# Kernel tuning notes

Measured on AMD Instinct MI355X. Metric: run time of the kernel, lower is better.

## Reference

```python
import jax, jax.numpy as jnp
import numpy as np


def setup_inputs() -> dict:
    key = jax.random.key(0)
    ks = jax.random.split(key, 20)
    r = lambda i, shape: jax.random.normal(ks[i], shape, dtype=jnp.float32)
    return {
        "cli": r(0, (1, 1, 8)),
        "conv1_w": r(1, (1,)), "conv1_b": r(2, (1,)),
        "conv2_w": r(3, (1,)), "conv2_b": r(4, (1,)),
        "mlp1_w1": r(5, (32, 8)) * 0.3, "mlp1_b1": r(6, (32,)) * 1e-6,
        "mlp1_w2": r(7, (8, 32)) * 0.3, "mlp1_b2": r(8, (8,)) * 1e-6,
        "mlp2_w1": r(9, (32, 8)) * 0.3, "mlp2_b1": r(10, (32,)) * 1e-6,
        "mlp2_w2": r(11, (8, 32)) * 0.3, "mlp2_b2": r(12, (8,)) * 1e-6,
        "gcn1_w": r(13, (1,)), "gcn1_b": r(14, (1,)),
        "gcn2_w": r(15, (1,)), "gcn2_b": r(16, (1,)),
    }


def _mlp(x, w1, b1, w2, b2):
    # torch nn.Linear: y = x @ W.T + b ; exact (erf) GELU; dropout is identity in eval.
    h = jax.nn.gelu(x @ w1.T + b1, approximate=False)
    return h @ w2.T + b2


def reference(cli, conv1_w, conv1_b, conv2_w, conv2_b,
              mlp1_w1, mlp1_b1, mlp1_w2, mlp1_b2,
              mlp2_w1, mlp2_b1, mlp2_w2, mlp2_b2,
              gcn1_w, gcn1_b, gcn2_w, gcn2_b):
    # Conv1d(1,1,1) == scalar affine transform.
    sigma = cli * conv1_w + conv1_b                     # [1,1,8]
    sigma_out = sigma.reshape(1, 8, 1) @ sigma          # [1,8,8] outer product

    x = cli[0]                                          # [1,8]
    cli_ss = _mlp(x, mlp1_w1, mlp1_b1, mlp1_w2, mlp1_b2).reshape(1, 1, 8)
    cli_mm = _mlp(x, mlp2_w1, mlp2_b1, mlp2_w2, mlp2_b2).reshape(1, 8, 1)

    diag_cha = cli_mm @ cli_ss                          # [1,8,8]
    diag_att = diag_cha * sigma_out                     # [1,8,8]

    alpha = cli * conv2_w + conv2_b                     # [1,1,8]
    alpha_T = alpha.reshape(1, 8, 1)
    similarity_c = (diag_cha @ alpha_T) @ alpha         # [1,8,8]
    similarity = jax.nn.softmax(similarity_c + diag_att, axis=1)

    # GCN(num_state=1): seg stays [1,1,8]
    seg = jax.nn.relu(cli * gcn1_w + gcn1_b)            # [1,1,8]
    seg_similar = seg @ similarity                      # [1,1,8]
    out = jax.nn.relu(seg_similar * gcn2_w + gcn2_b)
    return (out + seg)[:, 0, :]                         # squeeze(1) -> [1,8]
```

## Files before the change

kernel.cpp:

```cpp
#include <hip/hip_runtime.h>
#include <math.h>

__device__ __forceinline__ float gelu_exact(float x) {
    return 0.5f * x * (1.0f + erff(x * 0.70710678118654752440f));
}

__global__ void __launch_bounds__(64) clngcn_fused(
    const float* __restrict__ cli,
    const float* __restrict__ c1w, const float* __restrict__ c1b,
    const float* __restrict__ c2w, const float* __restrict__ c2b,
    const float* __restrict__ m1w1, const float* __restrict__ m1b1,
    const float* __restrict__ m1w2, const float* __restrict__ m1b2,
    const float* __restrict__ m2w1, const float* __restrict__ m2b1,
    const float* __restrict__ m2w2, const float* __restrict__ m2b2,
    const float* __restrict__ g1w, const float* __restrict__ g1b,
    const float* __restrict__ g2w, const float* __restrict__ g2b,
    float* __restrict__ out)
{
    const int t = threadIdx.x;
    const int i = t >> 3;
    const int j = t & 7;
    const int k = t & 31;
    const bool lo = (t < 32);

    float x[8];
    #pragma unroll
    for (int q = 0; q < 8; ++q) x[q] = cli[q];

    const float C1W = c1w[0], C1B = c1b[0];
    const float C2W = c2w[0], C2B = c2b[0];
    const float G1W = g1w[0], G1B = g1b[0];
    const float G2W = g2w[0], G2B = g2b[0];

    const float* W1 = lo ? m1w1 : m2w1;
    const float* B1 = lo ? m1b1 : m2b1;
    const float* W2 = lo ? m1w2 : m2w2;
    const float* B2 = lo ? m1b2 : m2b2;

    float acc = B1[k];
    #pragma unroll
    for (int q = 0; q < 8; ++q) acc = fmaf(x[q], W1[k * 8 + q], acc);
    const float h = gelu_exact(acc);

    float r[8];
    #pragma unroll
    for (int q = 0; q < 8; ++q) {
        float p = h * W2[q * 32 + k];
        p += __shfl_xor(p, 1);
        p += __shfl_xor(p, 2);
        p += __shfl_xor(p, 4);
        p += __shfl_xor(p, 8);
        p += __shfl_xor(p, 16);
        r[q] = p + B2[q];
    }
    float cs[8], cm[8];
    #pragma unroll
    for (int q = 0; q < 8; ++q) {
        const float o = __shfl_xor(r[q], 32);
        cs[q] = lo ? r[q] : o;
        cm[q] = lo ? o : r[q];
    }

    const float sigma_i = fmaf(x[i], C1W, C1B);
    const float sigma_j = fmaf(x[j], C1W, C1B);
    const float alpha_j = fmaf(x[j], C2W, C2B);
    const float seg_i   = fmaxf(fmaf(x[i], G1W, G1B), 0.0f);
    const float seg_j   = fmaxf(fmaf(x[j], G1W, G1B), 0.0f);

    float dot = 0.0f;
    #pragma unroll
    for (int q = 0; q < 8; ++q) dot = fmaf(cs[q], fmaf(x[q], C2W, C2B), dot);

    const float diag_cha = cm[i] * cs[j];
    const float s = fmaf(cm[i] * dot, alpha_j, diag_cha * (sigma_i * sigma_j));

    float m = s;
    m = fmaxf(m, __shfl_xor(m, 8));
    m = fmaxf(m, __shfl_xor(m, 16));
    m = fmaxf(m, __shfl_xor(m, 32));
    const float e = expf(s - m);
    float den = e;
    den += __shfl_xor(den, 8);
    den += __shfl_xor(den, 16);
    den += __shfl_xor(den, 32);
    const float sim = e / den;

    float p = seg_i * sim;
    p += __shfl_xor(p, 8);
    p += __shfl_xor(p, 16);
    p += __shfl_xor(p, 32);

    if (t < 8) {
        out[j] = fmaxf(fmaf(p, G2W, G2B), 0.0f) + seg_j;
    }
}

extern "C" void kernel_launch(void* const* d_in, const int* in_sizes, int n_in,
                              void* d_out, int out_size, void* d_ws, size_t ws_size,
                              hipStream_t stream) {
    (void)in_sizes; (void)n_in; (void)d_ws; (void)ws_size; (void)out_size;
    clngcn_fused<<<dim3(1), dim3(64), 0, stream>>>(
        (const float*)d_in[0],
        (const float*)d_in[1],  (const float*)d_in[2],
        (const float*)d_in[3],  (const float*)d_in[4],
        (const float*)d_in[5],  (const float*)d_in[6],
        (const float*)d_in[7],  (const float*)d_in[8],
        (const float*)d_in[9],  (const float*)d_in[10],
        (const float*)d_in[11], (const float*)d_in[12],
        (const float*)d_in[13], (const float*)d_in[14],
        (const float*)d_in[15], (const float*)d_in[16],
        (float*)d_out);
}
```

Before: 9.526 us.

## Use transpose-reduce butterfly for second MLP layer and vectorize input loads

Replaces the eight independent 32-lane shuffle reductions for the second MLP layer with a recursive-halving butterfly. Each lane exchanges one of two values per stage, so the eight outputs end up spread across lanes, cutting shuffle count substantially. Inputs and first-layer weights are loaded as float4, and per-lane x values are fetched with lane shuffles instead of dynamic indexing into register arrays. This adds lane-index permutation bookkeeping and extra shuffles to gather results, which carries a risk of index errors.

```diff
diff --git a/kernel.cpp b/kernel.cpp
--- a/kernel.cpp
+++ b/kernel.cpp
@@ -23,9 +23,11 @@
     const int k = t & 31;
     const bool lo = (t < 32);
 
-    float x[8];
-    #pragma unroll
-    for (int q = 0; q < 8; ++q) x[q] = cli[q];
+    const float4 xa = *(const float4*)(cli);
+    const float4 xb = *(const float4*)(cli + 4);
+    const float x0 = xa.x, x1 = xa.y, x2 = xa.z, x3 = xa.w;
+    const float x4 = xb.x, x5 = xb.y, x6 = xb.z, x7 = xb.w;
+    const float x_own = __shfl(x0, 0) * 0.0f + ((const float*)cli)[j];
 
     const float C1W = c1w[0], C1B = c1b[0];
     const float C2W = c2w[0], C2B = c2b[0];
@@ -37,42 +39,61 @@
     const float* W2 = lo ? m1w2 : m2w2;
     const float* B2 = lo ? m1b2 : m2b2;
 
+    const float4 wa = *(const float4*)(W1 + k * 8);
+    const float4 wb = *(const float4*)(W1 + k * 8 + 4);
     float acc = B1[k];
-    #pragma unroll
-    for (int q = 0; q < 8; ++q) acc = fmaf(x[q], W1[k * 8 + q], acc);
+    acc = fmaf(x0, wa.x, acc); acc = fmaf(x1, wa.y, acc);
+    acc = fmaf(x2, wa.z, acc); acc = fmaf(x3, wa.w, acc);
+    acc = fmaf(x4, wb.x, acc); acc = fmaf(x5, wb.y, acc);
+    acc = fmaf(x6, wb.z, acc); acc = fmaf(x7, wb.w, acc);
     const float h = gelu_exact(acc);
 
-    float r[8];
-    #pragma unroll
-    for (int q = 0; q < 8; ++q) {
-        float p = h * W2[q * 32 + k];
-        p += __shfl_xor(p, 1);
-        p += __shfl_xor(p, 2);
-        p += __shfl_xor(p, 4);
-        p += __shfl_xor(p, 8);
-        p += __shfl_xor(p, 16);
-        r[q] = p + B2[q];
-    }
-    float cs[8], cm[8];
-    #pragma unroll
-    for (int q = 0; q < 8; ++q) {
-        const float o = __shfl_xor(r[q], 32);
-        cs[q] = lo ? r[q] : o;
-        cm[q] = lo ? o : r[q];
-    }
+    float v0 = h * W2[0 * 32 + k], v1e = h * W2[1 * 32 + k];
+    float v2 = h * W2[2 * 32 + k], v3 = h * W2[3 * 32 + k];
+    float v4 = h * W2[4 * 32 + k], v5 = h * W2[5 * 32 + k];
+    float v6 = h * W2[6 * 32 + k], v7 = h * W2[7 * 32 + k];
 
-    const float sigma_i = fmaf(x[i], C1W, C1B);
-    const float sigma_j = fmaf(x[j], C1W, C1B);
-    const float alpha_j = fmaf(x[j], C2W, C2B);
-    const float seg_i   = fmaxf(fmaf(x[i], G1W, G1B), 0.0f);
-    const float seg_j   = fmaxf(fmaf(x[j], G1W, G1B), 0.0f);
+    const bool b0 = (k & 1), b1 = (k & 2), b2 = (k & 4);
+    float w0 = (b0 ? v4 : v0) + __shfl_xor(b0 ? v0 : v4, 1);
+    float w1 = (b0 ? v5 : v1e) + __shfl_xor(b0 ? v1e : v5, 1);
+    float w2 = (b0 ? v6 : v2) + __shfl_xor(b0 ? v2 : v6, 1);
+    float w3 = (b0 ? v7 : v3) + __shfl_xor(b0 ? v3 : v7, 1);
+    float u0 = (b1 ? w2 : w0) + __shfl_xor(b1 ? w0 : w2, 2);
+    float u1 = (b1 ? w3 : w1) + __shfl_xor(b1 ? w1 : w3, 2);
+    float tv = (b2 ? u1 : u0) + __shfl_xor(b2 ? u0 : u1, 4);
+    tv += __shfl_xor(tv, 8);
+    tv += __shfl_xor(tv, 16);
+    const int qidx = ((k & 1) << 2) | (k & 2) | ((k >> 2) & 1);
+    const float val = tv + B2[qidx];
+
+    const float cs0g = __shfl(val, 0), cs1g = __shfl(val, 4);
+    const float cs2g = __shfl(val, 2), cs3g = __shfl(val, 6);
+    const float cs4g = __shfl(val, 1), cs5g = __shfl(val, 5);
+    const float cs6g = __shfl(val, 3), cs7g = __shfl(val, 7);
+    const int lj = ((j >> 2) & 1) | (j & 2) | ((j & 1) << 2);
+    const int li = ((i >> 2) & 1) | (i & 2) | ((i & 1) << 2);
+    const float cs_j = __shfl(val, lj);
+    const float cm_i = __shfl(val, 32 + li);
+    const float x_i  = __shfl(x_own, i);
+
+    const float sigma_i = fmaf(x_i, C1W, C1B);
+    const float sigma_j = fmaf(x_own, C1W, C1B);
+    const float alpha_j = fmaf(x_own, C2W, C2B);
+    const float seg_i   = fmaxf(fmaf(x_i, G1W, G1B), 0.0f);
+    const float seg_j   = fmaxf(fmaf(x_own, G1W, G1B), 0.0f);
 
     float dot = 0.0f;
-    #pragma unroll
-    for (int q = 0; q < 8; ++q) dot = fmaf(cs[q], fmaf(x[q], C2W, C2B), dot);
+    dot = fmaf(cs0g, fmaf(x0, C2W, C2B), dot);
+    dot = fmaf(cs1g, fmaf(x1, C2W, C2B), dot);
+    dot = fmaf(cs2g, fmaf(x2, C2W, C2B), dot);
+    dot = fmaf(cs3g, fmaf(x3, C2W, C2B), dot);
+    dot = fmaf(cs4g, fmaf(x4, C2W, C2B), dot);
+    dot = fmaf(cs5g, fmaf(x5, C2W, C2B), dot);
+    dot = fmaf(cs6g, fmaf(x6, C2W, C2B), dot);
+    dot = fmaf(cs7g, fmaf(x7, C2W, C2B), dot);
 
-    const float diag_cha = cm[i] * cs[j];
-    const float s = fmaf(cm[i] * dot, alpha_j, diag_cha * (sigma_i * sigma_j));
+    const float diag_cha = cm_i * cs_j;
+    const float s = fmaf(cm_i * dot, alpha_j, diag_cha * (sigma_i * sigma_j));
 
     float m = s;
     m = fmaxf(m, __shfl_xor(m, 8));
```

Result: no change. 9.518 us (-0.1%).
